# Performance work log

Measured on AMD Instinct MI355X. Metric: run time of the kernel, lower is better.

The kernel has to match this reference:

```python
import jax, jax.numpy as jnp
import numpy as np

N_HEAD = 16
ROPE_BASE = 10000.0


def _rope_tables(T, head_dim, dtype):
    # RotaryEmbedding(dim=head_dim//2): inv_freq over arange(0, dim, 2)/dim
    rot = head_dim // 2  # 32
    inv_freq = 1.0 / (ROPE_BASE ** (jnp.arange(0, rot, 2, dtype=jnp.float32) / rot))  # [rot/2]
    pos = jnp.arange(T, dtype=jnp.float32)
    freqs = jnp.outer(pos, inv_freq)                     # [T, rot/2]
    emb = jnp.concatenate([freqs, freqs], axis=-1)       # [T, rot]
    return jnp.cos(emb).astype(dtype), jnp.sin(emb).astype(dtype)


def _apply_rope(q, k, cos, sin):
    # q,k: [B,H,T,hd]; cos,sin: [T, hd//2] broadcast over B,H
    hd = q.shape[-1]
    half = hd // 2
    cos = cos[None, None]
    sin = sin[None, None]
    q1, q2 = q[..., :half], q[..., half:]
    k1, k2 = k[..., :half], k[..., half:]
    q_rot = jnp.concatenate([q1 * cos - q2 * sin, q2 * cos + q1 * sin], axis=-1)
    k_rot = jnp.concatenate([k1 * cos - k2 * sin, k2 * cos + k1 * sin], axis=-1)
    return q_rot, k_rot


def setup_inputs() -> dict:
    key = jax.random.key(0)
    ks = jax.random.split(key, 4)
    B, T, C = 4, 2048, 1024
    x = jax.random.normal(ks[0], (B, T, C), dtype=jnp.float32)
    W_attn = jax.random.normal(ks[1], (C, 3 * C), dtype=jnp.float32) * (1.0 / np.sqrt(C))
    b_attn = jnp.zeros((3 * C,), dtype=jnp.float32)
    W_proj = jax.random.normal(ks[2], (C, C), dtype=jnp.float32) * (1.0 / np.sqrt(C))
    b_proj = jnp.zeros((C,), dtype=jnp.float32)
    return {"x": x, "W_attn": W_attn, "b_attn": b_attn, "W_proj": W_proj, "b_proj": b_proj}


def reference(x, W_attn, b_attn, W_proj, b_proj):
    B, T, C = x.shape
    H = N_HEAD
    hd = C // H
    qkv = x @ W_attn + b_attn                            # [B,T,3C]
    q, k, v = jnp.split(qkv, 3, axis=-1)
    # [B,T,C] -> [B,H,T,hd]
    q = q.reshape(B, T, H, hd).transpose(0, 2, 1, 3)
    k = k.reshape(B, T, H, hd).transpose(0, 2, 1, 3)
    v = v.reshape(B, T, H, hd).transpose(0, 2, 1, 3)
    cos, sin = _rope_tables(T, hd, x.dtype)
    q, k = _apply_rope(q, k, cos, sin)
    att = jnp.einsum("bhqd,bhkd->bhqk", q, k) * (1.0 / np.sqrt(hd))
    causal = jnp.tril(jnp.ones((T, T), dtype=bool))
    att = jnp.where(causal[None, None], att, jnp.float32(-jnp.inf).astype(att.dtype))
    att = jax.nn.softmax(att, axis=-1)
    y = jnp.einsum("bhqk,bhkd->bhqd", att, v)            # [B,H,T,hd]
    y = y.transpose(0, 2, 1, 3).reshape(B, T, C)
    return y @ W_proj + b_proj
```

## Files before the change

### kernel.cpp

```cpp
#include <hip/hip_runtime.h>
#include <math.h>


typedef unsigned short u16;
typedef __bf16 bf16x8 __attribute__((ext_vector_type(8)));
typedef float f32x4 __attribute__((ext_vector_type(4)));
typedef float f32x16 __attribute__((ext_vector_type(16)));

#define QSCALE 0.18033688501389543f

__device__ __forceinline__ float b2f(u16 x) {
  union { unsigned u; float f; } c; c.u = ((unsigned)x) << 16; return c.f;
}
__device__ __forceinline__ u16 f2b(float f) {
  union { __bf16 h; u16 u; } c; c.h = (__bf16)f; return c.u;
}

#define GLOAD16(gp, lp)                                                  \
  __builtin_amdgcn_global_load_lds(                                      \
      (const __attribute__((address_space(1))) unsigned int*)(gp),       \
      (__attribute__((address_space(3))) unsigned int*)(lp), 16, 0, 0)

__global__ __launch_bounds__(256) void sentinel_k(u16* __restrict__ out, int n) {
  int i = blockIdx.x * 256 + threadIdx.x;
  if (i < n) out[i] = 0x4480;
}

__global__ __launch_bounds__(256) void transpose_f2b_k(const float* __restrict__ src,
                                                       u16* __restrict__ dst,
                                                       int R, int C) {
  __shared__ u16 tile[64][65];
  int tc = blockIdx.x * 64, tr = blockIdx.y * 64;
  int t = threadIdx.x;
  int rr = t >> 3;
  int c8 = (t & 7) * 8;
#pragma unroll
  for (int i = 0; i < 2; ++i) {
    int r = rr + i * 32;
    f32x4 p0 = *(const f32x4*)(src + (long)(tr + r) * C + tc + c8);
    f32x4 p1 = *(const f32x4*)(src + (long)(tr + r) * C + tc + c8 + 4);
#pragma unroll
    for (int j = 0; j < 4; ++j) {
      tile[r][c8 + j] = f2b(p0[j]);
      tile[r][c8 + 4 + j] = f2b(p1[j]);
    }
  }
  __syncthreads();
#pragma unroll
  for (int i = 0; i < 2; ++i) {
    int a = rr + i * 32;
    u16 vv[8];
#pragma unroll
    for (int j = 0; j < 8; ++j) vv[j] = tile[c8 + j][a];
    *(uint4*)(dst + (long)(tc + a) * R + tr + c8) = *(uint4*)vv;
  }
}

__global__ __launch_bounds__(256) void transpose_b_k(const u16* __restrict__ src,
                                                     u16* __restrict__ dst,
                                                     int R, int C,
                                                     long sBatch, long dBatch) {
  __shared__ u16 tile[64][65];
  src += (long)blockIdx.z * sBatch;
  dst += (long)blockIdx.z * dBatch;
  int tc = blockIdx.x * 64, tr = blockIdx.y * 64;
  int t = threadIdx.x;
  int rr = t >> 3;
  int c8 = (t & 7) * 8;
#pragma unroll
  for (int i = 0; i < 2; ++i) {
    int r = rr + i * 32;
    uint4 v = *(const uint4*)(src + (long)(tr + r) * C + tc + c8);
    u16 vv[8]; *(uint4*)vv = v;
#pragma unroll
    for (int j = 0; j < 8; ++j) tile[r][c8 + j] = vv[j];
  }
  __syncthreads();
#pragma unroll
  for (int i = 0; i < 2; ++i) {
    int a = rr + i * 32;
    u16 vv[8];
#pragma unroll
    for (int j = 0; j < 8; ++j) vv[j] = tile[c8 + j][a];
    *(uint4*)(dst + (long)(tc + a) * R + tr + c8) = *(uint4*)vv;
  }
}

__global__ void rope_table_k(float2* __restrict__ tab) {
  int i = blockIdx.x * 256 + threadIdx.x;
  if (i >= 2048 * 16) return;
  int t = i >> 4, f = i & 15;
  float invf = exp2f(-(float)f * (13.287712379549449f / 16.0f));
  float th = (float)t * invf;
  float s, c;
  sincosf(th, &s, &c);
  tab[i] = make_float2(c, s);
}

__global__ __launch_bounds__(256) void gemm_qkv_k(const float* __restrict__ A,
                                                  const u16* __restrict__ Bt,
                                                  const float* __restrict__ bias,
                                                  const float2* __restrict__ tab,
                                                  u16* __restrict__ out,
                                                  int M, int N, int K) {
  __shared__ u16 As[128 * 40];
  __shared__ u16 Bs[128 * 40];
  int tid = threadIdx.x, wid = tid >> 6, lane = tid & 63;
  int wr = wid >> 1, wc = wid & 1;
  long m0 = (long)blockIdx.x * 128, n0 = (long)blockIdx.y * 128;
  int r = lane & 15, g = lane >> 4;
  long arow = m0 + wid * 32 + (lane >> 2);
  int acol = (lane & 3) * 8;
  const float* Agf = A + arow * (long)K + acol;
  const u16* Bg = Bt + (n0 + wid * 32 + (lane >> 2)) * (long)K + acol;
  int lrow = wid * 32 + (lane >> 2);
  int lcol = acol;
  f32x4 acc[4][4] = {};
  int nk = K >> 5;
  for (int kt = 0; kt < nk; ++kt) {
    long ko = (long)kt * 32;
    f32x4 p0 = *(const f32x4*)(Agf + ko);
    f32x4 p1 = *(const f32x4*)(Agf + ko + 4);
    f32x4 p2 = *(const f32x4*)(Agf + ko + 16 * (long)K);
    f32x4 p3 = *(const f32x4*)(Agf + ko + 16 * (long)K + 4);
    u16 h0[8], h1[8];
#pragma unroll
    for (int j = 0; j < 4; ++j) {
      h0[j] = f2b(p0[j]); h0[4 + j] = f2b(p1[j]);
      h1[j] = f2b(p2[j]); h1[4 + j] = f2b(p3[j]);
    }
    uint4 a0 = *(uint4*)h0, a1 = *(uint4*)h1;
    uint4 b0 = *(const uint4*)(Bg + ko);
    uint4 b1 = *(const uint4*)(Bg + ko + 16 * (long)K);
    __syncthreads();
    *(uint4*)&As[lrow * 40 + lcol] = a0;
    *(uint4*)&As[(lrow + 16) * 40 + lcol] = a1;
    *(uint4*)&Bs[lrow * 40 + lcol] = b0;
    *(uint4*)&Bs[(lrow + 16) * 40 + lcol] = b1;
    __syncthreads();
    bf16x8 af[4], bfr[4];
#pragma unroll
    for (int mt = 0; mt < 4; ++mt)
      af[mt] = *(const bf16x8*)&As[(wr * 64 + mt * 16 + r) * 40 + g * 8];
#pragma unroll
    for (int nt = 0; nt < 4; ++nt)
      bfr[nt] = *(const bf16x8*)&Bs[(wc * 64 + nt * 16 + r) * 40 + g * 8];
#pragma unroll
    for (int mt = 0; mt < 4; ++mt)
#pragma unroll
      for (int nt = 0; nt < 4; ++nt)
        acc[mt][nt] = __builtin_amdgcn_mfma_f32_16x16x32_bf16(af[mt], bfr[nt], acc[mt][nt], 0, 0, 0);
  }
  int which = (int)(n0 >> 10);
  int hh = ((int)(n0 & 1023) >> 6) + wc;
  float bv[4];
#pragma unroll
  for (int nt = 0; nt < 4; ++nt) bv[nt] = bias[n0 + wc * 64 + nt * 16 + r];
#pragma unroll
  for (int mt = 0; mt < 4; ++mt) {
#pragma unroll
    for (int e = 0; e < 4; ++e) {
      long row = m0 + wr * 64 + mt * 16 + g * 4 + e;
      long bb = row >> 11;
      int tt = (int)row & 2047;
      float v0 = acc[mt][0][e] + bv[0];
      float v1 = acc[mt][1][e] + bv[1];
      float v2 = acc[mt][2][e] + bv[2];
      float v3 = acc[mt][3][e] + bv[3];
      if (which < 2) {
        float2 cs = tab[tt * 16 + r];
        float r0 = v0 * cs.x - v2 * cs.y, r2 = v2 * cs.x + v0 * cs.y;
        float r1 = v1 * cs.x - v3 * cs.y, r3 = v3 * cs.x + v1 * cs.y;
        if (which == 0) { r0 *= QSCALE; r1 *= QSCALE; r2 *= QSCALE; r3 *= QSCALE; }
        v0 = r0; v1 = r1; v2 = r2; v3 = r3;
      }
      u16* op = out + (long)which * 8388608 + (((bb * 16 + hh) * 2048 + tt) << 6);
      op[r] = f2b(v0);
      op[16 + r] = f2b(v1);
      op[32 + r] = f2b(v2);
      op[48 + r] = f2b(v3);
    }
  }
}

__global__ __launch_bounds__(256) void gemm_proj_k(const u16* __restrict__ A,
                                                   const u16* __restrict__ Bt,
                                                   const float* __restrict__ bias,
                                                   float* __restrict__ out,
                                                   int M, int N, int K) {
  __shared__ u16 As[128 * 32];
  __shared__ u16 Bs[128 * 32];
  int tid = threadIdx.x, wid = tid >> 6, lane = tid & 63;
  int wr = wid >> 1, wc = wid & 1;
  long m0 = (long)blockIdx.x * 128, n0 = (long)blockIdx.y * 128;
  int r = lane & 15, g = lane >> 4;
  const u16* Ag = A + (m0 + wid * 32 + (lane >> 2)) * (long)K + (lane & 3) * 8;
  const u16* Bg = Bt + (n0 + wid * 32 + (lane >> 2)) * (long)K + (lane & 3) * 8;
  u16* AsW = As + wid * 1024;
  u16* BsW = Bs + wid * 1024;
  f32x4 acc[4][4] = {};
  int nk = K >> 5;
  for (int kt = 0; kt < nk; ++kt) {
    long ko = (long)kt * 32;
    GLOAD16(Ag + ko, AsW);
    GLOAD16(Ag + ko + 16 * (long)K, AsW + 512);
    GLOAD16(Bg + ko, BsW);
    GLOAD16(Bg + ko + 16 * (long)K, BsW + 512);
    __syncthreads();
    bf16x8 af[4], bfr[4];
#pragma unroll
    for (int mt = 0; mt < 4; ++mt)
      af[mt] = *(const bf16x8*)&As[(wr * 64 + mt * 16 + r) * 32 + g * 8];
#pragma unroll
    for (int nt = 0; nt < 4; ++nt)
      bfr[nt] = *(const bf16x8*)&Bs[(wc * 64 + nt * 16 + r) * 32 + g * 8];
#pragma unroll
    for (int mt = 0; mt < 4; ++mt)
#pragma unroll
      for (int nt = 0; nt < 4; ++nt)
        acc[mt][nt] = __builtin_amdgcn_mfma_f32_16x16x32_bf16(af[mt], bfr[nt], acc[mt][nt], 0, 0, 0);
    __syncthreads();
  }
#pragma unroll
  for (int nt = 0; nt < 4; ++nt) {
    long col = n0 + wc * 64 + nt * 16 + r;
    float bvv = bias[col];
#pragma unroll
    for (int mt = 0; mt < 4; ++mt)
#pragma unroll
      for (int e = 0; e < 4; ++e) {
        long row = m0 + wr * 64 + mt * 16 + g * 4 + e;
        out[row * N + col] = acc[mt][nt][e] + bvv;
      }
  }
}

__device__ __forceinline__ void pk_exchange(const f32x16& p, bf16x8& af0, bf16x8& af1) {
  unsigned w0, w1, w2, w3, w4, w5, w6, w7;
  asm("v_cvt_pk_bf16_f32 %0, %1, %2" : "=v"(w0) : "v"(p[0]), "v"(p[1]));
  asm("v_cvt_pk_bf16_f32 %0, %1, %2" : "=v"(w1) : "v"(p[2]), "v"(p[3]));
  asm("v_cvt_pk_bf16_f32 %0, %1, %2" : "=v"(w2) : "v"(p[4]), "v"(p[5]));
  asm("v_cvt_pk_bf16_f32 %0, %1, %2" : "=v"(w3) : "v"(p[6]), "v"(p[7]));
  asm("v_cvt_pk_bf16_f32 %0, %1, %2" : "=v"(w4) : "v"(p[8]), "v"(p[9]));
  asm("v_cvt_pk_bf16_f32 %0, %1, %2" : "=v"(w5) : "v"(p[10]), "v"(p[11]));
  asm("v_cvt_pk_bf16_f32 %0, %1, %2" : "=v"(w6) : "v"(p[12]), "v"(p[13]));
  asm("v_cvt_pk_bf16_f32 %0, %1, %2" : "=v"(w7) : "v"(p[14]), "v"(p[15]));
  asm("v_permlane32_swap_b32 %0, %1" : "+v"(w0), "+v"(w2));
  asm("v_permlane32_swap_b32 %0, %1" : "+v"(w1), "+v"(w3));
  asm("v_permlane32_swap_b32 %0, %1" : "+v"(w4), "+v"(w6));
  asm("v_permlane32_swap_b32 %0, %1" : "+v"(w5), "+v"(w7));
  union { unsigned u[4]; bf16x8 v; } c0, c1;
  c0.u[0] = w0; c0.u[1] = w1; c0.u[2] = w2; c0.u[3] = w3;
  c1.u[0] = w4; c1.u[1] = w5; c1.u[2] = w6; c1.u[3] = w7;
  af0 = c0.v;
  af1 = c1.v;
}

__global__ __launch_bounds__(256) void attn_k(const u16* __restrict__ Qg,
                                              const u16* __restrict__ Kg,
                                              const u16* __restrict__ VgT,
                                              u16* __restrict__ Y) {
  __shared__ u16 Ks[64 * 72];
  __shared__ u16 Vt[64 * 72];
  int qb = 15 - (int)blockIdx.y;
  int bh = blockIdx.x;
  int b = bh >> 4, h = bh & 15;
  long base = (long)bh * (2048 * 64);
  int tid = threadIdx.x, wid = tid >> 6;
  int lane = tid & 63, l31 = lane & 31, hi = lane >> 5;
  int q0 = qb * 128 + wid * 32;
  int endS = (q0 + 31) >> 6;
  int ktMax = 2 * qb + 1;
  int srow = tid >> 3, sch = (tid & 7) * 8;
  const u16* kSrc0 = Kg + base + (long)srow * 64 + sch;
  const u16* kSrc1 = kSrc0 + 32 * 64;
  const u16* vSrc0 = VgT + base + (long)srow * 2048 + sch;
  const u16* vSrc1 = vSrc0 + 32 * 2048;
  int sOff0 = srow * 72 + sch;
  int sOff1 = (srow + 32) * 72 + sch;
  bf16x8 qf[4];
  {
    const u16* qp = Qg + base + (long)(q0 + l31) * 64 + hi * 8;
#pragma unroll
    for (int s4 = 0; s4 < 4; ++s4) qf[s4] = *(const bf16x8*)(qp + s4 * 16);
  }
  f32x16 acc0 = {}, acc1 = {};
  float mrow = -INFINITY, lrow = 0.f;
  uint4 rk0 = *(const uint4*)kSrc0;
  uint4 rk1 = *(const uint4*)kSrc1;
  uint4 rv0 = *(const uint4*)vSrc0;
  uint4 rv1 = *(const uint4*)vSrc1;
  for (int kt = 0; kt <= ktMax; ++kt) {
    __syncthreads();
    *(uint4*)&Ks[sOff0] = rk0;
    *(uint4*)&Ks[sOff1] = rk1;
    *(uint4*)&Vt[sOff0] = rv0;
    *(uint4*)&Vt[sOff1] = rv1;
    __syncthreads();
    if (kt < ktMax) {
      long ko = (long)(kt + 1) * 4096;
      long vo = (long)(kt + 1) * 64;
      rk0 = *(const uint4*)(kSrc0 + ko);
      rk1 = *(const uint4*)(kSrc1 + ko);
      rv0 = *(const uint4*)(vSrc0 + vo);
      rv1 = *(const uint4*)(vSrc1 + vo);
    }
    if (kt > endS) continue;
    f32x16 st[2];
    __builtin_amdgcn_s_setprio(1);
#pragma unroll
    for (int ct = 0; ct < 2; ++ct) {
      f32x16 z = {};
#pragma unroll
      for (int s4 = 0; s4 < 4; ++s4) {
        bf16x8 kf = *(const bf16x8*)&Ks[(ct * 32 + l31) * 72 + s4 * 16 + hi * 8];
        z = __builtin_amdgcn_mfma_f32_32x32x16_bf16(kf, qf[s4], z, 0, 0, 0);
      }
      st[ct] = z;
    }
    __builtin_amdgcn_s_setprio(0);
    if (kt == endS) {
      int qg = q0 + l31;
#pragma unroll
      for (int ct = 0; ct < 2; ++ct)
#pragma unroll
        for (int reg = 0; reg < 16; ++reg) {
          int kg = kt * 64 + ct * 32 + (reg & 3) + 8 * (reg >> 2) + 4 * hi;
          if (kg > qg) st[ct][reg] = -INFINITY;
        }
    }
    float t8[8];
#pragma unroll
    for (int i = 0; i < 8; ++i)
      t8[i] = fmaxf(fmaxf(st[0][i], st[0][i + 8]), fmaxf(st[1][i], st[1][i + 8]));
#pragma unroll
    for (int i = 0; i < 4; ++i) t8[i] = fmaxf(t8[i], t8[i + 4]);
    float pm = fmaxf(fmaxf(t8[0], t8[1]), fmaxf(t8[2], t8[3]));
    pm = fmaxf(pm, __shfl_xor(pm, 32));
    if (__any(pm > mrow + 8.0f)) {
      float mn = fmaxf(mrow, pm);
      float alpha = exp2f(mrow - mn);
      mrow = mn;
      lrow *= alpha;
#pragma unroll
      for (int reg = 0; reg < 16; ++reg) {
        float aB = __shfl(alpha, (reg & 3) + 8 * (reg >> 2) + 4 * hi);
        acc0[reg] *= aB;
        acc1[reg] *= aB;
      }
    }
    float s8[8];
#pragma unroll
    for (int i = 0; i < 8; ++i) s8[i] = 0.f;
#pragma unroll
    for (int ct = 0; ct < 2; ++ct)
#pragma unroll
      for (int reg = 0; reg < 16; ++reg) {
        float p = exp2f(st[ct][reg] - mrow);
        st[ct][reg] = p;
        s8[reg & 7] += p;
      }
#pragma unroll
    for (int i = 0; i < 4; ++i) s8[i] += s8[i + 4];
    float rs = (s8[0] + s8[1]) + (s8[2] + s8[3]);
    rs += __shfl_xor(rs, 32);
    lrow += rs;
#pragma unroll
    for (int ct = 0; ct < 2; ++ct) {
      bf16x8 af[2];
      pk_exchange(st[ct], af[0], af[1]);
      __builtin_amdgcn_s_setprio(1);
#pragma unroll
      for (int ks = 0; ks < 2; ++ks) {
        bf16x8 vf0 = *(const bf16x8*)&Vt[l31 * 72 + ct * 32 + ks * 16 + hi * 8];
        bf16x8 vf1 = *(const bf16x8*)&Vt[(32 + l31) * 72 + ct * 32 + ks * 16 + hi * 8];
        acc0 = __builtin_amdgcn_mfma_f32_32x32x16_bf16(af[ks], vf0, acc0, 0, 0, 0);
        acc1 = __builtin_amdgcn_mfma_f32_32x32x16_bf16(af[ks], vf1, acc1, 0, 0, 0);
      }
      __builtin_amdgcn_s_setprio(0);
    }
  }
  float rinv = 1.0f / lrow;
#pragma unroll
  for (int reg = 0; reg < 16; ++reg) {
    int crow = (reg & 3) + 8 * (reg >> 2) + 4 * hi;
    float rB = __shfl(rinv, crow);
    long orow = (long)(b * 2048 + q0 + crow) * 1024 + h * 64;
    Y[orow + l31] = f2b(acc0[reg] * rB);
    Y[orow + 32 + l31] = f2b(acc1[reg] * rB);
  }
}

extern "C" void kernel_launch(void* const* d_in, const int* in_sizes, int n_in,
                              void* d_out, int out_size, void* d_ws, size_t ws_size,
                              hipStream_t stream) {
  const float* x  = (const float*)d_in[0];
  const float* Wa = (const float*)d_in[1];
  const float* ba = (const float*)d_in[2];
  const float* Wp = (const float*)d_in[3];
  const float* bp = (const float*)d_in[4];

  if (ws_size < 67108864ULL) {
    sentinel_k<<<dim3((out_size + 255) / 256), 256, 0, stream>>>((u16*)d_out, out_size);
    return;
  }

  u16* ws  = (u16*)d_ws;
  u16* Qg  = ws;
  u16* Kg  = ws + 8388608;
  u16* Vg  = ws + 16777216;
  u16* Yb  = ws + 16777216;
  u16* WaT = ws + 25165824;
  float2* tab = (float2*)(ws + 28311552);
  u16* VgT = ws + 25165824;
  u16* WpT = ws;

  transpose_f2b_k<<<dim3(48, 16), 256, 0, stream>>>(Wa, WaT, 1024, 3072);
  rope_table_k<<<dim3(128), 256, 0, stream>>>(tab);
  gemm_qkv_k<<<dim3(64, 24), 256, 0, stream>>>(x, WaT, ba, tab, Qg, 8192, 3072, 1024);
  transpose_b_k<<<dim3(1, 32, 64), 256, 0, stream>>>(Vg, VgT, 2048, 64, 131072L, 131072L);
  attn_k<<<dim3(64, 16), 256, 0, stream>>>(Qg, Kg, VgT, Yb);
  transpose_f2b_k<<<dim3(16, 16), 256, 0, stream>>>(Wp, WpT, 1024, 1024);
  gemm_proj_k<<<dim3(64, 8), 256, 0, stream>>>(Yb, WpT, bp, (float*)d_out, 8192, 1024, 1024);
}
```

Measured before the change: 210.3 us.

## Double attention block to 256 query rows with 8 waves and reorder query tiles

The attention kernel now runs 512 threads (8 waves) per block covering 256 query rows instead of 128. Each thread stages one K row chunk and one V row chunk per tile, so the shared-memory K/V tiles serve twice as many query waves and global K/V traffic per query drops. Query blocks are launched in a fixed permuted order to spread causal workload. In exchange there are half as many blocks, a larger per-block causal imbalance (waves with early rows idle through more tiles), and more waves contending at each barrier.

Result: faster. 199.1 us (-5.3%).

```diff
diff --git a/kernel.cpp b/kernel.cpp
--- a/kernel.cpp
+++ b/kernel.cpp
@@ -256,28 +256,26 @@
   af1 = c1.v;
 }
 
-__global__ __launch_bounds__(256) void attn_k(const u16* __restrict__ Qg,
+__global__ __launch_bounds__(512) void attn_k(const u16* __restrict__ Qg,
                                               const u16* __restrict__ Kg,
                                               const u16* __restrict__ VgT,
                                               u16* __restrict__ Y) {
   __shared__ u16 Ks[64 * 72];
   __shared__ u16 Vt[64 * 72];
-  int qb = 15 - (int)blockIdx.y;
+  const int qmap[8] = {7, 5, 6, 4, 0, 2, 1, 3};
+  int qb = qmap[blockIdx.y];
   int bh = blockIdx.x;
   int b = bh >> 4, h = bh & 15;
   long base = (long)bh * (2048 * 64);
   int tid = threadIdx.x, wid = tid >> 6;
   int lane = tid & 63, l31 = lane & 31, hi = lane >> 5;
-  int q0 = qb * 128 + wid * 32;
+  int q0 = qb * 256 + wid * 32;
   int endS = (q0 + 31) >> 6;
-  int ktMax = 2 * qb + 1;
+  int ktMax = 4 * qb + 3;
   int srow = tid >> 3, sch = (tid & 7) * 8;
-  const u16* kSrc0 = Kg + base + (long)srow * 64 + sch;
-  const u16* kSrc1 = kSrc0 + 32 * 64;
-  const u16* vSrc0 = VgT + base + (long)srow * 2048 + sch;
-  const u16* vSrc1 = vSrc0 + 32 * 2048;
-  int sOff0 = srow * 72 + sch;
-  int sOff1 = (srow + 32) * 72 + sch;
+  const u16* kSrc = Kg + base + (long)srow * 64 + sch;
+  const u16* vSrc = VgT + base + (long)srow * 2048 + sch;
+  int sOff = srow * 72 + sch;
   bf16x8 qf[4];
   {
     const u16* qp = Qg + base + (long)(q0 + l31) * 64 + hi * 8;
@@ -286,24 +284,16 @@
   }
   f32x16 acc0 = {}, acc1 = {};
   float mrow = -INFINITY, lrow = 0.f;
-  uint4 rk0 = *(const uint4*)kSrc0;
-  uint4 rk1 = *(const uint4*)kSrc1;
-  uint4 rv0 = *(const uint4*)vSrc0;
-  uint4 rv1 = *(const uint4*)vSrc1;
+  uint4 rk = *(const uint4*)kSrc;
+  uint4 rv = *(const uint4*)vSrc;
   for (int kt = 0; kt <= ktMax; ++kt) {
     __syncthreads();
-    *(uint4*)&Ks[sOff0] = rk0;
-    *(uint4*)&Ks[sOff1] = rk1;
-    *(uint4*)&Vt[sOff0] = rv0;
-    *(uint4*)&Vt[sOff1] = rv1;
+    *(uint4*)&Ks[sOff] = rk;
+    *(uint4*)&Vt[sOff] = rv;
     __syncthreads();
     if (kt < ktMax) {
-      long ko = (long)(kt + 1) * 4096;
-      long vo = (long)(kt + 1) * 64;
-      rk0 = *(const uint4*)(kSrc0 + ko);
-      rk1 = *(const uint4*)(kSrc1 + ko);
-      rv0 = *(const uint4*)(vSrc0 + vo);
-      rv1 = *(const uint4*)(vSrc1 + vo);
+      rk = *(const uint4*)(kSrc + (long)(kt + 1) * 4096);
+      rv = *(const uint4*)(vSrc + (long)(kt + 1) * 64);
     }
     if (kt > endS) continue;
     f32x16 st[2];
@@ -419,7 +409,7 @@
   rope_table_k<<<dim3(128), 256, 0, stream>>>(tab);
   gemm_qkv_k<<<dim3(64, 24), 256, 0, stream>>>(x, WaT, ba, tab, Qg, 8192, 3072, 1024);
   transpose_b_k<<<dim3(1, 32, 64), 256, 0, stream>>>(Vg, VgT, 2048, 64, 131072L, 131072L);
-  attn_k<<<dim3(64, 16), 256, 0, stream>>>(Qg, Kg, VgT, Yb);
+  attn_k<<<dim3(64, 8), 512, 0, stream>>>(Qg, Kg, VgT, Yb);
   transpose_f2b_k<<<dim3(16, 16), 256, 0, stream>>>(Wp, WpT, 1024, 1024);
   gemm_proj_k<<<dim3(64, 8), 256, 0, stream>>>(Yb, WpT, bp, (float*)d_out, 8192, 1024, 1024);
 }
```
